# Performance work log

Measured on AMD Instinct MI355X. Metric: run time of the kernel, lower is better.

## Reference

```python
import jax, jax.numpy as jnp
import numpy as np

N = 100000      # nodes
E = 800000      # edges (avg degree 8)
F = 5           # num_node_features
D = 128         # embed_dim
H = 4           # heads
HD = D // H     # per-head dim = 32
H1, H2 = 64, 128  # mlp hidden dims


def _mlp(x, W1, b1, W2, b2, W3, b3):
    h = jax.nn.relu(x @ W1 + b1)
    h = jax.nn.relu(h @ W2 + b2)
    return h @ W3 + b3


def setup_inputs() -> dict:
    key = jax.random.key(0)
    ks = jax.random.split(key, 24)
    g = lambda i, shape: (jax.random.normal(ks[i], shape, dtype=jnp.float32) * 0.05)
    z = lambda d: jnp.zeros((d,), dtype=jnp.float32)
    return {
        "x": jax.random.normal(ks[0], (N, F), dtype=jnp.float32),
        "edge_index": jax.random.randint(ks[1], (2, E), 0, N),
        # mlp_prep: F -> 64 -> 128 -> D
        "prep_W1": g(2, (F, H1)),  "prep_b1": z(H1),
        "prep_W2": g(3, (H1, H2)), "prep_b2": z(H2),
        "prep_W3": g(4, (H2, D)),  "prep_b3": z(D),
        # mlp_update: D -> 64 -> 128 -> D
        "upd_W1": g(5, (D, H1)),   "upd_b1": z(H1),
        "upd_W2": g(6, (H1, H2)),  "upd_b2": z(H2),
        "upd_W3": g(7, (H2, D)),   "upd_b3": z(D),
        # TransformerConv projections (heads=4, per-head 32, concat -> D)
        "q_W": g(8, (D, D)),  "q_b": z(D),
        "k_W": g(9, (D, D)),  "k_b": z(D),
        "v_W": g(10, (D, D)), "v_b": z(D),
        "skip_W": g(11, (D, D)), "skip_b": z(D),
    }


def _transformer_conv(x, edge_index, q_W, q_b, k_W, k_b, v_W, v_b, skip_W, skip_b):
    # PyG TransformerConv: messages flow src=edge_index[0] -> dst=edge_index[1]
    src, dst = edge_index[0], edge_index[1]
    q = (x @ q_W + q_b).reshape(N, H, HD)
    k = (x @ k_W + k_b).reshape(N, H, HD)
    v = (x @ v_W + v_b).reshape(N, H, HD)
    scale = 1.0 / np.sqrt(HD).astype(np.float32)
    # per-edge attention logits [E, H]
    score = jnp.einsum('ehd,ehd->eh', q[dst], k[src]) * scale
    # segment softmax over incoming edges of each destination node
    m = jax.ops.segment_max(score, dst, num_segments=N)          # [N, H]
    e = jnp.exp(score - m[dst])                                  # [E, H]
    denom = jax.ops.segment_sum(e, dst, num_segments=N)         # [N, H]
    alpha = e / denom[dst]                                       # [E, H]
    # scatter-aggregate weighted values
    agg = jax.ops.segment_sum(alpha[..., None] * v[src], dst, num_segments=N)  # [N, H, HD]
    return agg.reshape(N, H * HD) + (x @ skip_W + skip_b)


def reference(x, edge_index,
              prep_W1, prep_b1, prep_W2, prep_b2, prep_W3, prep_b3,
              upd_W1, upd_b1, upd_W2, upd_b2, upd_W3, upd_b3,
              q_W, q_b, k_W, k_b, v_W, v_b, skip_W, skip_b):
    h_init = _mlp(x, prep_W1, prep_b1, prep_W2, prep_b2, prep_W3, prep_b3)
    h = _transformer_conv(h_init, edge_index, q_W, q_b, k_W, k_b, v_W, v_b, skip_W, skip_b)
    return h + _mlp(h, upd_W1, upd_b1, upd_W2, upd_b2, upd_W3, upd_b3)
```

## Files before the change

kernel.cpp:

```cpp
#include <hip/hip_runtime.h>
#include <hip/hip_bf16.h>

#define N_  100000
#define F_  5
#define D_  128
#define H_  4
#define HD_ 32
#define E_  800000

typedef __attribute__((ext_vector_type(8))) short bf16x8;
typedef __attribute__((ext_vector_type(4))) float f32x4;

__device__ __forceinline__ unsigned short f2bf(float f) {
  unsigned u = __float_as_uint(f);
  u += 0x7FFF + ((u >> 16) & 1);
  return (unsigned short)(u >> 16);
}

__device__ __forceinline__ unsigned pk2(float a, float b) {
  __hip_bfloat162 h = __float22bfloat162_rn(make_float2(a, b));
  return *(unsigned*)&h;
}

__device__ __forceinline__ float2 bf2f2(unsigned u) {
  float2 r;
  r.x = __uint_as_float(u << 16);
  r.y = __uint_as_float(u & 0xffff0000u);
  return r;
}

__device__ __forceinline__ float rowsum16(float x) {
  x += __int_as_float(__builtin_amdgcn_update_dpp(0, __float_as_int(x), 0x128, 0xF, 0xF, false));
  x += __int_as_float(__builtin_amdgcn_update_dpp(0, __float_as_int(x), 0x124, 0xF, 0xF, false));
  x += __int_as_float(__builtin_amdgcn_update_dpp(0, __float_as_int(x), 0x122, 0xF, 0xF, false));
  x += __int_as_float(__builtin_amdgcn_update_dpp(0, __float_as_int(x), 0x121, 0xF, 0xF, false));
  return x;
}

template<int K, int M>
__device__ __forceinline__ void wconv_one(const float* __restrict__ W,
                                          unsigned short* __restrict__ WT,
                                          int idx) {
  const int r = idx & 7;
  const int l = (idx >> 3) & 15;
  const int rest = idx >> 7;
  const int kq = rest % (K / 8);
  const int i  = rest / (K / 8);
  WT[idx] = f2bf(W[(kq * 8 + r) * M + i * 16 + l]);
}

#define WCONV_NB 480
#define SCAN_NB ((N_ + 255) / 256)

__global__ __launch_bounds__(256) void k_wconv_all(
    const float* __restrict__ w0, const float* __restrict__ w1,
    const float* __restrict__ w2, const float* __restrict__ w3,
    const float* __restrict__ w4, const float* __restrict__ w5,
    const float* __restrict__ w6, const float* __restrict__ w7,
    const float* __restrict__ w8, unsigned short* __restrict__ WT,
    int* __restrict__ deg)
{
  if (blockIdx.x >= WCONV_NB) {
    const int i = (blockIdx.x - WCONV_NB) * 256 + threadIdx.x;
    if (i < N_) deg[i] = 0;
    return;
  }
  const int idx = blockIdx.x * 256 + threadIdx.x;
  if (idx < 8192)        wconv_one<64, 128>(w0, WT,          idx);
  else if (idx < 24576)  wconv_one<128,128>(w1, WT + 8192,   idx - 8192);
  else if (idx < 40960)  wconv_one<128,128>(w2, WT + 24576,  idx - 24576);
  else if (idx < 57344)  wconv_one<128,128>(w3, WT + 40960,  idx - 40960);
  else if (idx < 73728)  wconv_one<128,128>(w4, WT + 57344,  idx - 57344);
  else if (idx < 90112)  wconv_one<128,128>(w5, WT + 73728,  idx - 73728);
  else if (idx < 98304)  wconv_one<128, 64>(w6, WT + 90112,  idx - 90112);
  else if (idx < 106496) wconv_one<64, 128>(w7, WT + 98304,  idx - 98304);
  else                   wconv_one<128,128>(w8, WT + 106496, idx - 106496);
}

template<int K, int M>
__device__ __forceinline__ void gemm_frag(const unsigned short* sX,
                                          const unsigned short* __restrict__ WT,
                                          f32x4 (*acc)[4],
                                          int wr, int wc, int l16, int kg)
{
  constexpr int SX = K + 8;
  constexpr int IF = M / 32;
  #pragma unroll
  for (int i = 0; i < IF; ++i)
    #pragma unroll
    for (int j = 0; j < 4; ++j) acc[i][j] = (f32x4){0.f, 0.f, 0.f, 0.f};
  #pragma unroll
  for (int k0 = 0; k0 < K; k0 += 32) {
    const int kq = k0 / 8 + kg;
    bf16x8 aw[IF];
    #pragma unroll
    for (int i = 0; i < IF; ++i)
      aw[i] = *(const bf16x8*)&WT[(((wr * IF + i) * (K / 8) + kq) * 16 + l16) * 8];
    #pragma unroll
    for (int j = 0; j < 4; ++j) {
      const bf16x8 bx = *(const bf16x8*)&sX[(wc * 64 + j * 16 + l16) * SX + k0 + kg * 8];
      #pragma unroll
      for (int i = 0; i < IF; ++i)
        acc[i][j] = __builtin_amdgcn_mfma_f32_16x16x32_bf16(aw[i], bx, acc[i][j], 0, 0, 0);
    }
  }
}

template<int M, bool RELU, int SXO>
__device__ __forceinline__ void acc_to_lds(unsigned short* sY, f32x4 (*acc)[4],
                                           const float* __restrict__ bias,
                                           int wr, int wc, int l16, int kg)
{
  constexpr int IF = M / 32;
  float4 b4[IF];
  #pragma unroll
  for (int i = 0; i < IF; ++i)
    b4[i] = *(const float4*)&bias[(wr * IF + i) * 16 + kg * 4];
  #pragma unroll
  for (int j = 0; j < 4; ++j) {
    const int row = wc * 64 + j * 16 + l16;
    #pragma unroll
    for (int i = 0; i < IF; ++i) {
      const int f0 = (wr * IF + i) * 16 + kg * 4;
      float ox = acc[i][j][0] + b4[i].x, oy = acc[i][j][1] + b4[i].y;
      float oz = acc[i][j][2] + b4[i].z, ow = acc[i][j][3] + b4[i].w;
      if constexpr (RELU) {
        ox = fmaxf(ox, 0.f); oy = fmaxf(oy, 0.f);
        oz = fmaxf(oz, 0.f); ow = fmaxf(ow, 0.f);
      }
      uint2 p;
      p.x = pk2(ox, oy);
      p.y = pk2(oz, ow);
      *(uint2*)&sY[row * SXO + f0] = p;
    }
  }
}

__global__ __launch_bounds__(256) void k_prep_proj(
    const float* __restrict__ x,
    const float* __restrict__ pW1, const float* __restrict__ pb1,
    const unsigned short* __restrict__ wt_p2, const float* __restrict__ pb2,
    const unsigned short* __restrict__ wt_p3, const float* __restrict__ pb3,
    const unsigned short* __restrict__ wt_q, const float* __restrict__ qb,
    const unsigned short* __restrict__ wt_k, const float* __restrict__ kb,
    const unsigned short* __restrict__ wt_v, const float* __restrict__ vb,
    const unsigned short* __restrict__ wt_s, const float* __restrict__ sb,
    unsigned short* __restrict__ q16, unsigned short* __restrict__ k16,
    unsigned short* __restrict__ v16, float* __restrict__ out)
{
  __shared__ __align__(16) unsigned short bufA[128 * 72];
  __shared__ __align__(16) unsigned short bufB[128 * 136];

  const int t = threadIdx.x;
  const int node0 = blockIdx.x * 128;
  const int lane = t & 63;
  const int w  = t >> 6;
  const int wr = w >> 1, wc = w & 1;
  const int l16 = lane & 15, kg = lane >> 4;

  float* sxs = (float*)bufB;
  float* sw1 = (float*)bufB + 640;
  {
    const long gbase = (long)node0 * F_;
    for (int i = t; i < 128 * F_; i += 256) {
      const long g = gbase + i;
      sxs[i] = (g < (long)N_ * F_) ? x[g] : 0.f;
    }
    for (int i = t; i < 384; i += 256)
      sw1[i] = (i < 320) ? pW1[i] : pb1[i - 320];
  }
  __syncthreads();

  {
    const int n = t >> 1;
    const int half = (t & 1) * 32;
    float xr[F_];
    #pragma unroll
    for (int k = 0; k < F_; ++k) xr[k] = sxs[n * F_ + k];
    const float* sb1 = sw1 + 320;
    #pragma unroll
    for (int q = 0; q < 8; ++q) {
      float o[4];
      #pragma unroll
      for (int jj = 0; jj < 4; ++jj) {
        const int f = half + q * 4 + jj;
        float a = sb1[f];
        #pragma unroll
        for (int k = 0; k < F_; ++k) a = fmaf(xr[k], sw1[k * 64 + f], a);
        o[jj] = fmaxf(a, 0.f);
      }
      uint2 pkd;
      pkd.x = pk2(o[0], o[1]);
      pkd.y = pk2(o[2], o[3]);
      *(uint2*)&bufA[n * 72 + half + q * 4] = pkd;
    }
  }
  __syncthreads();

  f32x4 acc[4][4];

  gemm_frag<64, 128>(bufA, wt_p2, acc, wr, wc, l16, kg);
  acc_to_lds<128, true, 136>(bufB, acc, pb2, wr, wc, l16, kg);
  __syncthreads();

  gemm_frag<128, 128>(bufB, wt_p3, acc, wr, wc, l16, kg);
  __syncthreads();
  acc_to_lds<128, false, 136>(bufB, acc, pb3, wr, wc, l16, kg);
  __syncthreads();

  {
    const unsigned short* wtsP[3] = {wt_q, wt_k, wt_v};
    const float* bsP[3] = {qb, kb, vb};
    unsigned short* ysP[3] = {q16, k16, v16};
    #pragma unroll
    for (int ws = 0; ws < 3; ++ws) {
      gemm_frag<128, 128>(bufB, wtsP[ws], acc, wr, wc, l16, kg);
      const float* __restrict__ bias = bsP[ws];
      unsigned short* __restrict__ Yb = ysP[ws];
      float4 b4[4];
      #pragma unroll
      for (int i = 0; i < 4; ++i)
        b4[i] = *(const float4*)&bias[(wr * 4 + i) * 16 + kg * 4];
      #pragma unroll
      for (int j = 0; j < 4; ++j) {
        const int node = node0 + wc * 64 + j * 16 + l16;
        if (node >= N_) continue;
        #pragma unroll
        for (int i = 0; i < 4; ++i) {
          const int f0 = (wr * 4 + i) * 16 + kg * 4;
          uint2 ob;
          ob.x = pk2(acc[i][j][0] + b4[i].x, acc[i][j][1] + b4[i].y);
          ob.y = pk2(acc[i][j][2] + b4[i].z, acc[i][j][3] + b4[i].w);
          *(uint2*)&Yb[(long)node * D_ + f0] = ob;
        }
      }
    }
  }

  gemm_frag<128, 128>(bufB, wt_s, acc, wr, wc, l16, kg);
  {
    float4 b4[4];
    #pragma unroll
    for (int i = 0; i < 4; ++i)
      b4[i] = *(const float4*)&sb[(wr * 4 + i) * 16 + kg * 4];
    #pragma unroll
    for (int j = 0; j < 4; ++j) {
      const int node = node0 + wc * 64 + j * 16 + l16;
      if (node >= N_) continue;
      #pragma unroll
      for (int i = 0; i < 4; ++i) {
        const int f0 = (wr * 4 + i) * 16 + kg * 4;
        float4 o = make_float4(acc[i][j][0] + b4[i].x, acc[i][j][1] + b4[i].y,
                               acc[i][j][2] + b4[i].z, acc[i][j][3] + b4[i].w);
        *(float4*)&out[(long)node * D_ + f0] = o;
      }
    }
  }
}

__global__ __launch_bounds__(256) void k_update(
    const unsigned short* __restrict__ wt_u1, const float* __restrict__ ub1,
    const unsigned short* __restrict__ wt_u2, const float* __restrict__ ub2,
    const unsigned short* __restrict__ wt_u3, const float* __restrict__ ub3,
    float* __restrict__ out)
{
  __shared__ __align__(16) unsigned short bufA[128 * 72];
  __shared__ __align__(16) unsigned short bufB[128 * 136];

  const int t = threadIdx.x;
  const int node0 = blockIdx.x * 128;
  const int lane = t & 63;
  const int w  = t >> 6;
  const int wr = w >> 1, wc = w & 1;
  const int l16 = lane & 15, kg = lane >> 4;

  #pragma unroll
  for (int i = 0; i < 16; ++i) {
    const int g = t + 256 * i;
    const int row = g >> 5;
    const int kc  = g & 31;
    const int node = node0 + row;
    float4 xv = (node < N_) ? ((const float4*)out)[(long)node * 32 + kc]
                            : make_float4(0.f, 0.f, 0.f, 0.f);
    uint2 p;
    p.x = pk2(xv.x, xv.y);
    p.y = pk2(xv.z, xv.w);
    *(uint2*)&bufB[row * 136 + kc * 4] = p;
  }
  __syncthreads();

  f32x4 acc[4][4];

  gemm_frag<128, 64>(bufB, wt_u1, acc, wr, wc, l16, kg);
  acc_to_lds<64, true, 72>(bufA, acc, ub1, wr, wc, l16, kg);
  __syncthreads();

  gemm_frag<64, 128>(bufA, wt_u2, acc, wr, wc, l16, kg);
  acc_to_lds<128, true, 136>(bufB, acc, ub2, wr, wc, l16, kg);
  __syncthreads();

  gemm_frag<128, 128>(bufB, wt_u3, acc, wr, wc, l16, kg);
  {
    float4 b4[4];
    #pragma unroll
    for (int i = 0; i < 4; ++i)
      b4[i] = *(const float4*)&ub3[(wr * 4 + i) * 16 + kg * 4];
    #pragma unroll
    for (int j = 0; j < 4; ++j) {
      const int node = node0 + wc * 64 + j * 16 + l16;
      if (node >= N_) continue;
      #pragma unroll
      for (int i = 0; i < 4; ++i) {
        const int f0 = (wr * 4 + i) * 16 + kg * 4;
        const float4 r = *(const float4*)&out[(long)node * D_ + f0];
        float4 o = make_float4(acc[i][j][0] + b4[i].x + r.x,
                               acc[i][j][1] + b4[i].y + r.y,
                               acc[i][j][2] + b4[i].z + r.z,
                               acc[i][j][3] + b4[i].w + r.w);
        *(float4*)&out[(long)node * D_ + f0] = o;
      }
    }
  }
}

__global__ __launch_bounds__(256) void k_hist(const int* __restrict__ ei,
                                              int* __restrict__ deg) {
  int e = blockIdx.x * 256 + threadIdx.x;
  if (e < E_) atomicAdd(&deg[ei[E_ + e]], 1);
}

__global__ __launch_bounds__(256) void k_scan1(const int* __restrict__ deg,
                                               int* __restrict__ off,
                                               int* __restrict__ bsum) {
  __shared__ int s[256];
  const int t = threadIdx.x;
  const int i = blockIdx.x * 256 + t;
  const int v = (i < N_) ? deg[i] : 0;
  s[t] = v;
  __syncthreads();
  #pragma unroll
  for (int o = 1; o < 256; o <<= 1) {
    int u = (t >= o) ? s[t - o] : 0;
    __syncthreads();
    s[t] += u;
    __syncthreads();
  }
  if (i < N_) off[i] = s[t] - v;
  if (t == 255) bsum[blockIdx.x] = s[255];
}

__global__ __launch_bounds__(512) void k_scan2(int* __restrict__ bsum) {
  __shared__ int s[512];
  const int t = threadIdx.x;
  const int v = (t < SCAN_NB) ? bsum[t] : 0;
  s[t] = v;
  __syncthreads();
  #pragma unroll
  for (int o = 1; o < 512; o <<= 1) {
    int u = (t >= o) ? s[t - o] : 0;
    __syncthreads();
    s[t] += u;
    __syncthreads();
  }
  if (t < SCAN_NB) bsum[t] = s[t] - v;
}

__global__ __launch_bounds__(256) void k_scan3(int* __restrict__ off,
                                               const int* __restrict__ bsum,
                                               int* __restrict__ cur) {
  const int i = blockIdx.x * 256 + threadIdx.x;
  if (i < N_) {
    const int o = off[i] + bsum[blockIdx.x];
    off[i] = o;
    cur[i] = o;
  }
}

__global__ __launch_bounds__(256) void k_fill(const int* __restrict__ ei,
                                              int* __restrict__ cur,
                                              int* __restrict__ esrc) {
  int e = blockIdx.x * 256 + threadIdx.x;
  if (e < E_) {
    int src = ei[e], dst = ei[E_ + e];
    int pos = atomicAdd(&cur[dst], 1);
    esrc[pos] = src;
  }
}

__global__ __launch_bounds__(256) void k_attn(
    const int* __restrict__ esrc, const int* __restrict__ off,
    const int* __restrict__ deg,
    const unsigned short* __restrict__ q,
    const unsigned short* __restrict__ kbuf,
    const unsigned short* __restrict__ vbuf,
    float* __restrict__ out)
{
  const int node = blockIdx.x * 4 + (threadIdx.x >> 6);
  const int lane = threadIdx.x & 63;
  if (node >= N_) return;

  const int start = off[node];
  const int cnt   = deg[node];
  const float C = 0.17677669529663687f * 1.4426950408889634f;

  const float2 qv = bf2f2(*(const unsigned*)&q[(long)node * D_ + 2 * lane]);
  const float qx = qv.x * C, qy = qv.y * C;

  float m = -__builtin_inff(), l = 0.f, a0 = 0.f, a1 = 0.f;

  const int pairs = cnt >> 1;
  if (pairs > 0) {
    int sa = esrc[start], sb = esrc[start + 1];
    unsigned kua = *(const unsigned*)&kbuf[(long)sa * D_ + 2 * lane];
    unsigned kub = *(const unsigned*)&kbuf[(long)sb * D_ + 2 * lane];
    unsigned vua = *(const unsigned*)&vbuf[(long)sa * D_ + 2 * lane];
    unsigned vub = *(const unsigned*)&vbuf[(long)sb * D_ + 2 * lane];

    for (int p = 1; ; ++p) {
      const unsigned cka = kua, ckb = kub, cva = vua, cvb = vub;
      const bool more = p < pairs;
      if (more) {
        const int i = start + 2 * p;
        sa = esrc[i];
        sb = esrc[i + 1];
        kua = *(const unsigned*)&kbuf[(long)sa * D_ + 2 * lane];
        kub = *(const unsigned*)&kbuf[(long)sb * D_ + 2 * lane];
        vua = *(const unsigned*)&vbuf[(long)sa * D_ + 2 * lane];
        vub = *(const unsigned*)&vbuf[(long)sb * D_ + 2 * lane];
      }

      const float2 ka = bf2f2(cka);
      const float2 kb2 = bf2f2(ckb);
      float pa = qx * ka.x + qy * ka.y;
      float pb = qx * kb2.x + qy * kb2.y;
      pa = rowsum16(pa);
      pb = rowsum16(pb);

      const float2 va = bf2f2(cva);
      const float2 vb2 = bf2f2(cvb);
      const float mn = fmaxf(m, fmaxf(pa, pb));
      const float s  = __builtin_amdgcn_exp2f(m - mn);
      const float ea = __builtin_amdgcn_exp2f(pa - mn);
      const float eb = __builtin_amdgcn_exp2f(pb - mn);
      l  = fmaf(l, s, ea + eb);
      a0 = fmaf(a0, s, fmaf(ea, va.x, eb * vb2.x));
      a1 = fmaf(a1, s, fmaf(ea, va.y, eb * vb2.y));
      m = mn;

      if (!more) break;
    }
  }

  if (cnt & 1) {
    const int i = start + (cnt & ~1);
    const int src = esrc[i];
    const unsigned ku = *(const unsigned*)&kbuf[(long)src * D_ + 2 * lane];
    const unsigned vu = *(const unsigned*)&vbuf[(long)src * D_ + 2 * lane];
    const float2 kf = bf2f2(ku);
    float p = qx * kf.x + qy * kf.y;
    p = rowsum16(p);

    const float2 vf = bf2f2(vu);
    const float mn = fmaxf(m, p);
    const float s  = __builtin_amdgcn_exp2f(m - mn);
    const float e  = __builtin_amdgcn_exp2f(p - mn);
    l  = fmaf(l, s, e);
    a0 = fmaf(a0, s, e * vf.x);
    a1 = fmaf(a1, s, e * vf.y);
    m = mn;
  }

  const float inv = (l > 0.f) ? (1.0f / l) : 0.f;
  float2* op = (float2*)&out[(long)node * D_ + 2 * lane];
  float2 cv = *op;
  cv.x += a0 * inv;
  cv.y += a1 * inv;
  *op = cv;
}

extern "C" void kernel_launch(void* const* d_in, const int* in_sizes, int n_in,
                              void* d_out, int out_size, void* d_ws, size_t ws_size,
                              hipStream_t stream) {
  const float* x   = (const float*)d_in[0];
  const int*   ei  = (const int*)d_in[1];
  const float* pW1 = (const float*)d_in[2];  const float* pb1 = (const float*)d_in[3];
  const float* pW2 = (const float*)d_in[4];  const float* pb2 = (const float*)d_in[5];
  const float* pW3 = (const float*)d_in[6];  const float* pb3 = (const float*)d_in[7];
  const float* uW1 = (const float*)d_in[8];  const float* ub1 = (const float*)d_in[9];
  const float* uW2 = (const float*)d_in[10]; const float* ub2 = (const float*)d_in[11];
  const float* uW3 = (const float*)d_in[12]; const float* ub3 = (const float*)d_in[13];
  const float* qW  = (const float*)d_in[14]; const float* qb  = (const float*)d_in[15];
  const float* kW  = (const float*)d_in[16]; const float* kb  = (const float*)d_in[17];
  const float* vW  = (const float*)d_in[18]; const float* vb  = (const float*)d_in[19];
  const float* sW  = (const float*)d_in[20]; const float* sb  = (const float*)d_in[21];

  float* out = (float*)d_out;
  float* ws  = (float*)d_ws;

  const long ND = (long)N_ * D_;
  unsigned short* q16 = (unsigned short*)(ws + ND);
  unsigned short* k16 = (unsigned short*)(ws + 2 * ND);
  unsigned short* v16 = (unsigned short*)(ws + 3 * ND);

  unsigned short* wtb = (unsigned short*)(ws + 4 * ND);
  unsigned short* wt_p2 = wtb;
  unsigned short* wt_p3 = wtb + 8192;
  unsigned short* wt_q  = wtb + 24576;
  unsigned short* wt_k  = wtb + 40960;
  unsigned short* wt_v  = wtb + 57344;
  unsigned short* wt_s  = wtb + 73728;
  unsigned short* wt_u1 = wtb + 90112;
  unsigned short* wt_u2 = wtb + 98304;
  unsigned short* wt_u3 = wtb + 106496;

  int* deg  = (int*)ws;
  int* off  = deg + N_;
  int* cur  = off + N_;
  int* esrc = cur + N_;
  int* bsum = esrc + E_;

  const int gT = (N_ + 127) / 128;

  k_wconv_all<<<WCONV_NB + SCAN_NB, 256, 0, stream>>>(
      pW2, pW3, qW, kW, vW, sW, uW1, uW2, uW3, wtb, deg);

  k_hist <<<(E_ + 255) / 256, 256, 0, stream>>>(ei, deg);
  k_scan1<<<SCAN_NB, 256, 0, stream>>>(deg, off, bsum);
  k_scan2<<<1, 512, 0, stream>>>(bsum);
  k_scan3<<<SCAN_NB, 256, 0, stream>>>(off, bsum, cur);
  k_fill <<<(E_ + 255) / 256, 256, 0, stream>>>(ei, cur, esrc);

  k_prep_proj<<<gT, 256, 0, stream>>>(
      x, pW1, pb1, wt_p2, pb2, wt_p3, pb3,
      wt_q, qb, wt_k, kb, wt_v, vb, wt_s, sb,
      q16, k16, v16, out);

  k_attn<<<(N_ + 3) / 4, 256, 0, stream>>>(esrc, off, deg, q16, k16, v16, out);

  k_update<<<gT, 256, 0, stream>>>(wt_u1, ub1, wt_u2, ub2, wt_u3, ub3, out);
}
```

Baseline: 372.1 us.

## Split attention edges across wave halves and merge scan2/scan3 kernels

The attention kernel now lets each half of a 64-lane wave process alternating edges, with each lane holding 4 channels (8-lane head reductions), and merges the two partial online-softmax states through a cross-half shuffle at the end. Each half runs a loop over its own edge stream with prefetch one edge ahead. Separately, the single-block scan2 and scan3 kernels are fused: each block sums the preceding block totals itself and adds that prefix. This removes one launch but adds redundant reads of the block sums. The attention change aims to raise memory-level parallelism and cut loop iterations, at the cost of masked tail work and a final merge step.

```diff
diff --git a/kernel.cpp b/kernel.cpp
--- a/kernel.cpp
+++ b/kernel.cpp
@@ -29,11 +29,10 @@
   return r;
 }
 
-__device__ __forceinline__ float rowsum16(float x) {
-  x += __int_as_float(__builtin_amdgcn_update_dpp(0, __float_as_int(x), 0x128, 0xF, 0xF, false));
-  x += __int_as_float(__builtin_amdgcn_update_dpp(0, __float_as_int(x), 0x124, 0xF, 0xF, false));
-  x += __int_as_float(__builtin_amdgcn_update_dpp(0, __float_as_int(x), 0x122, 0xF, 0xF, false));
-  x += __int_as_float(__builtin_amdgcn_update_dpp(0, __float_as_int(x), 0x121, 0xF, 0xF, false));
+__device__ __forceinline__ float rowsum8(float x) {
+  x += __int_as_float(__builtin_amdgcn_update_dpp(0, __float_as_int(x), 0x0B1, 0xF, 0xF, false));
+  x += __int_as_float(__builtin_amdgcn_update_dpp(0, __float_as_int(x), 0x04E, 0xF, 0xF, false));
+  x += __int_as_float(__builtin_amdgcn_update_dpp(0, __float_as_int(x), 0x141, 0xF, 0xF, false));
   return x;
 }
 
@@ -349,28 +348,25 @@
   if (t == 255) bsum[blockIdx.x] = s[255];
 }
 
-__global__ __launch_bounds__(512) void k_scan2(int* __restrict__ bsum) {
-  __shared__ int s[512];
+__global__ __launch_bounds__(256) void k_scan23(int* __restrict__ off,
+                                                const int* __restrict__ bsum,
+                                                int* __restrict__ cur) {
+  __shared__ int sacc[256];
   const int t = threadIdx.x;
-  const int v = (t < SCAN_NB) ? bsum[t] : 0;
-  s[t] = v;
-  __syncthreads();
-  #pragma unroll
-  for (int o = 1; o < 512; o <<= 1) {
-    int u = (t >= o) ? s[t - o] : 0;
+  const int bid = blockIdx.x;
+  int s = 0;
+  for (int j = t; j < bid; j += 256) s += bsum[j];
+  sacc[t] = s;
+  __syncthreads();
+  #pragma unroll
+  for (int o = 128; o > 0; o >>= 1) {
+    if (t < o) sacc[t] += sacc[t + o];
     __syncthreads();
-    s[t] += u;
-    __syncthreads();
-  }
-  if (t < SCAN_NB) bsum[t] = s[t] - v;
-}
-
-__global__ __launch_bounds__(256) void k_scan3(int* __restrict__ off,
-                                               const int* __restrict__ bsum,
-                                               int* __restrict__ cur) {
-  const int i = blockIdx.x * 256 + threadIdx.x;
+  }
+  const int prefix = sacc[0];
+  const int i = bid * 256 + t;
   if (i < N_) {
-    const int o = off[i] + bsum[blockIdx.x];
+    const int o = off[i] + prefix;
     off[i] = o;
     cur[i] = o;
   }
@@ -401,81 +397,88 @@
 
   const int start = off[node];
   const int cnt   = deg[node];
+  const int end   = start + cnt;
+  const int h = lane >> 5;
+  const int c = lane & 31;
   const float C = 0.17677669529663687f * 1.4426950408889634f;
 
-  const float2 qv = bf2f2(*(const unsigned*)&q[(long)node * D_ + 2 * lane]);
-  const float qx = qv.x * C, qy = qv.y * C;
-
-  float m = -__builtin_inff(), l = 0.f, a0 = 0.f, a1 = 0.f;
-
-  const int pairs = cnt >> 1;
-  if (pairs > 0) {
-    int sa = esrc[start], sb = esrc[start + 1];
-    unsigned kua = *(const unsigned*)&kbuf[(long)sa * D_ + 2 * lane];
-    unsigned kub = *(const unsigned*)&kbuf[(long)sb * D_ + 2 * lane];
-    unsigned vua = *(const unsigned*)&vbuf[(long)sa * D_ + 2 * lane];
-    unsigned vub = *(const unsigned*)&vbuf[(long)sb * D_ + 2 * lane];
-
-    for (int p = 1; ; ++p) {
-      const unsigned cka = kua, ckb = kub, cva = vua, cvb = vub;
-      const bool more = p < pairs;
+  const uint2 qu = *(const uint2*)&q[(long)node * D_ + 4 * c];
+  const float2 q01 = bf2f2(qu.x), q23 = bf2f2(qu.y);
+  const float qx0 = q01.x * C, qx1 = q01.y * C;
+  const float qx2 = q23.x * C, qx3 = q23.y * C;
+
+  float m = -__builtin_inff(), l = 0.f;
+  float a0 = 0.f, a1 = 0.f, a2 = 0.f, a3 = 0.f;
+
+  const int P = (cnt + 1) >> 1;
+  if (P > 0) {
+    int e = start + h;
+    bool v_cur = e < end;
+    int i_cur = esrc[v_cur ? e : start];
+    const int e1 = e + 2;
+    bool v_nxt = e1 < end;
+    int i_nxt = esrc[v_nxt ? e1 : start];
+
+    uint2 kc = *(const uint2*)&kbuf[(long)i_cur * D_ + 4 * c];
+    uint2 vc = *(const uint2*)&vbuf[(long)i_cur * D_ + 4 * c];
+
+    for (int p = 0; ; ++p) {
+      const bool more = (p + 1) < P;
+      uint2 kn, vn;
+      int i_n2 = 0;
+      bool v_n2 = false;
       if (more) {
-        const int i = start + 2 * p;
-        sa = esrc[i];
-        sb = esrc[i + 1];
-        kua = *(const unsigned*)&kbuf[(long)sa * D_ + 2 * lane];
-        kub = *(const unsigned*)&kbuf[(long)sb * D_ + 2 * lane];
-        vua = *(const unsigned*)&vbuf[(long)sa * D_ + 2 * lane];
-        vub = *(const unsigned*)&vbuf[(long)sb * D_ + 2 * lane];
+        kn = *(const uint2*)&kbuf[(long)i_nxt * D_ + 4 * c];
+        vn = *(const uint2*)&vbuf[(long)i_nxt * D_ + 4 * c];
+        const int e2 = start + 2 * (p + 2) + h;
+        v_n2 = e2 < end;
+        i_n2 = esrc[v_n2 ? e2 : start];
       }
 
-      const float2 ka = bf2f2(cka);
-      const float2 kb2 = bf2f2(ckb);
-      float pa = qx * ka.x + qy * ka.y;
-      float pb = qx * kb2.x + qy * kb2.y;
-      pa = rowsum16(pa);
-      pb = rowsum16(pb);
-
-      const float2 va = bf2f2(cva);
-      const float2 vb2 = bf2f2(cvb);
-      const float mn = fmaxf(m, fmaxf(pa, pb));
-      const float s  = __builtin_amdgcn_exp2f(m - mn);
-      const float ea = __builtin_amdgcn_exp2f(pa - mn);
-      const float eb = __builtin_amdgcn_exp2f(pb - mn);
-      l  = fmaf(l, s, ea + eb);
-      a0 = fmaf(a0, s, fmaf(ea, va.x, eb * vb2.x));
-      a1 = fmaf(a1, s, fmaf(ea, va.y, eb * vb2.y));
+      const float2 k01 = bf2f2(kc.x), k23 = bf2f2(kc.y);
+      float ps = fmaf(qx0, k01.x, fmaf(qx1, k01.y, fmaf(qx2, k23.x, qx3 * k23.y)));
+      ps = rowsum8(ps);
+      ps = v_cur ? ps : -__builtin_inff();
+
+      const float mn = fmaxf(m, ps);
+      const float s  = __builtin_amdgcn_exp2f(fmaxf(m  - mn, -200.f));
+      const float ee = __builtin_amdgcn_exp2f(fmaxf(ps - mn, -200.f));
+      const float2 v01 = bf2f2(vc.x), v23 = bf2f2(vc.y);
+      l  = fmaf(l,  s, ee);
+      a0 = fmaf(a0, s, ee * v01.x);
+      a1 = fmaf(a1, s, ee * v01.y);
+      a2 = fmaf(a2, s, ee * v23.x);
+      a3 = fmaf(a3, s, ee * v23.y);
       m = mn;
 
       if (!more) break;
-    }
-  }
-
-  if (cnt & 1) {
-    const int i = start + (cnt & ~1);
-    const int src = esrc[i];
-    const unsigned ku = *(const unsigned*)&kbuf[(long)src * D_ + 2 * lane];
-    const unsigned vu = *(const unsigned*)&vbuf[(long)src * D_ + 2 * lane];
-    const float2 kf = bf2f2(ku);
-    float p = qx * kf.x + qy * kf.y;
-    p = rowsum16(p);
-
-    const float2 vf = bf2f2(vu);
-    const float mn = fmaxf(m, p);
-    const float s  = __builtin_amdgcn_exp2f(m - mn);
-    const float e  = __builtin_amdgcn_exp2f(p - mn);
-    l  = fmaf(l, s, e);
-    a0 = fmaf(a0, s, e * vf.x);
-    a1 = fmaf(a1, s, e * vf.y);
-    m = mn;
-  }
-
-  const float inv = (l > 0.f) ? (1.0f / l) : 0.f;
-  float2* op = (float2*)&out[(long)node * D_ + 2 * lane];
-  float2 cv = *op;
-  cv.x += a0 * inv;
-  cv.y += a1 * inv;
-  *op = cv;
+      v_cur = v_nxt; kc = kn; vc = vn;
+      v_nxt = v_n2;  i_nxt = i_n2;
+    }
+  }
+
+  const float mB = __shfl_xor(m, 32);
+  const float lB = __shfl_xor(l, 32);
+  const float b0 = __shfl_xor(a0, 32);
+  const float b1 = __shfl_xor(a1, 32);
+  const float b2 = __shfl_xor(a2, 32);
+  const float b3 = __shfl_xor(a3, 32);
+
+  const float mm = fmaxf(m, mB);
+  const float sA = __builtin_amdgcn_exp2f(fmaxf(m  - mm, -200.f));
+  const float sB = __builtin_amdgcn_exp2f(fmaxf(mB - mm, -200.f));
+  const float L  = fmaf(l, sA, lB * sB);
+
+  if (h == 0 && L > 0.f) {
+    const float inv = 1.0f / L;
+    float4* op = (float4*)&out[(long)node * D_ + 4 * c];
+    float4 cv = *op;
+    cv.x += fmaf(a0, sA, b0 * sB) * inv;
+    cv.y += fmaf(a1, sA, b1 * sB) * inv;
+    cv.z += fmaf(a2, sA, b2 * sB) * inv;
+    cv.w += fmaf(a3, sA, b3 * sB) * inv;
+    *op = cv;
+  }
 }
 
 extern "C" void kernel_launch(void* const* d_in, const int* in_sizes, int n_in,
@@ -524,11 +527,10 @@
   k_wconv_all<<<WCONV_NB + SCAN_NB, 256, 0, stream>>>(
       pW2, pW3, qW, kW, vW, sW, uW1, uW2, uW3, wtb, deg);
 
-  k_hist <<<(E_ + 255) / 256, 256, 0, stream>>>(ei, deg);
-  k_scan1<<<SCAN_NB, 256, 0, stream>>>(deg, off, bsum);
-  k_scan2<<<1, 512, 0, stream>>>(bsum);
-  k_scan3<<<SCAN_NB, 256, 0, stream>>>(off, bsum, cur);
-  k_fill <<<(E_ + 255) / 256, 256, 0, stream>>>(ei, cur, esrc);
+  k_hist  <<<(E_ + 255) / 256, 256, 0, stream>>>(ei, deg);
+  k_scan1 <<<SCAN_NB, 256, 0, stream>>>(deg, off, bsum);
+  k_scan23<<<SCAN_NB, 256, 0, stream>>>(off, bsum, cur);
+  k_fill  <<<(E_ + 255) / 256, 256, 0, stream>>>(ei, cur, esrc);
 
   k_prep_proj<<<gT, 256, 0, stream>>>(
       x, pW1, pb1, wt_p2, pb2, wt_p3, pb3,
```

Result: faster. 357.8 us (-3.8%).
